# Optimization experiments

Measured on AMD Instinct MI355X. Metric: run time of the kernel, lower is better.

## Reference

```python
import jax, jax.numpy as jnp
import numpy as np

N, E = 50000, 800000
IN, EIN, HID, OUT = 128, 64, 256, 256
L, H = 3, 4
D = HID // H  # per-head out_feats


def setup_inputs() -> dict:
    key = jax.random.key(0)
    ks = jax.random.split(key, 20)
    s = 0.02
    return {
        "h": jax.random.normal(ks[0], (N, IN), jnp.float32),
        "efeat": jax.random.normal(ks[1], (E, EIN), jnp.float32),
        "src": jax.random.randint(ks[2], (E,), 0, N, jnp.int32),
        "dst": jax.random.randint(ks[3], (E,), 0, N, jnp.int32),
        "enc_w": jax.random.normal(ks[4], (IN, HID), jnp.float32) * s,
        "enc_b": jnp.zeros((HID,), jnp.float32),
        "eenc_w": jax.random.normal(ks[5], (EIN, HID), jnp.float32) * s,
        "eenc_b": jnp.zeros((HID,), jnp.float32),
        "Wn": jax.random.normal(ks[6], (L, HID, HID), jnp.float32) * s,
        "We": jax.random.normal(ks[7], (L, HID, HID), jnp.float32) * s,
        "al": jax.random.normal(ks[8], (L, H, D), jnp.float32) * s,
        "ar": jax.random.normal(ks[9], (L, H, D), jnp.float32) * s,
        "ae": jax.random.normal(ks[10], (L, H, D), jnp.float32) * s,
        "ln_g": jnp.ones((L, HID), jnp.float32),
        "ln_b": jnp.zeros((L, HID), jnp.float32),
        "out_w": jax.random.normal(ks[11], (HID, OUT), jnp.float32) * s,
        "out_b": jnp.zeros((OUT,), jnp.float32),
    }


def reference(h, efeat, src, dst, enc_w, enc_b, eenc_w, eenc_b,
              Wn, We, al, ar, ae, ln_g, ln_b, out_w, out_b):
    # Dropout layers act as identity (eval mode).
    n = h.shape[0]
    x = h @ enc_w + enc_b                      # [N, HID] node encoder
    ef = efeat @ eenc_w + eenc_b               # [E, HID] edge encoder
    nl, nh, nd = al.shape
    for l in range(nl):
        res = x
        feat = (x @ Wn[l]).reshape(n, nh, nd)          # [N,H,D]
        eft = (ef @ We[l]).reshape(-1, nh, nd)         # [E,H,D]
        el = jnp.sum(feat * al[l], axis=-1)            # [N,H]
        er = jnp.sum(feat * ar[l], axis=-1)            # [N,H]
        ee = jnp.sum(eft * ae[l], axis=-1)             # [E,H]
        e = jax.nn.leaky_relu(el[src] + er[dst] + ee, 0.2)  # [E,H]
        # edge softmax over incoming edges of each dst node
        m = jax.lax.stop_gradient(jax.ops.segment_max(e, dst, num_segments=n))
        a = jnp.exp(e - m[dst])
        ssum = jax.ops.segment_sum(a, dst, num_segments=n)
        alpha = a / ssum[dst]                          # [E,H]
        agg = jax.ops.segment_sum(alpha[:, :, None] * feat[src], dst,
                                  num_segments=n)      # [N,H,D]
        x = jax.nn.relu(agg.reshape(n, nh * nd))
        y = x + res
        mu = jnp.mean(y, axis=-1, keepdims=True)
        var = jnp.var(y, axis=-1, keepdims=True)
        x = (y - mu) / jnp.sqrt(var + 1e-5) * ln_g[l] + ln_b[l]
    return x @ out_w + out_b
```

## Files before the change

kernel.cpp:

```cpp
#include <hip/hip_runtime.h>
#include <math.h>


typedef __attribute__((ext_vector_type(8))) short bf16x8;
typedef __attribute__((ext_vector_type(4))) float f32x4;

__device__ __forceinline__ ushort f2b(float f) {
    unsigned u; __builtin_memcpy(&u, &f, 4);
    unsigned r = u + 0x7FFF + ((u >> 16) & 1);
    return (ushort)(r >> 16);
}
__device__ __forceinline__ float b2f(ushort u) {
    unsigned x = (unsigned)u << 16;
    float f; __builtin_memcpy(&f, &x, 4);
    return f;
}

__global__ void k_deg(const int* __restrict__ dst, int* __restrict__ deg, int E) {
    int e = blockIdx.x * 256 + threadIdx.x;
    if (e < E) atomicAdd(&deg[dst[e]], 1);
}

__global__ void k_bsum(const int* __restrict__ deg, int* __restrict__ bsum, int n) {
    __shared__ int wsum[4];
    int tid = threadIdx.x;
    int idx = blockIdx.x * 1024 + tid * 4;
    int4 v = make_int4(0, 0, 0, 0);
    if (idx + 3 < n) v = *(const int4*)(deg + idx);
    else {
        if (idx + 0 < n) v.x = deg[idx + 0];
        if (idx + 1 < n) v.y = deg[idx + 1];
        if (idx + 2 < n) v.z = deg[idx + 2];
    }
    int s = v.x + v.y + v.z + v.w;
#pragma unroll
    for (int off = 32; off; off >>= 1) s += __shfl_down(s, off, 64);
    if ((tid & 63) == 0) wsum[tid >> 6] = s;
    __syncthreads();
    if (tid == 0) bsum[blockIdx.x] = wsum[0] + wsum[1] + wsum[2] + wsum[3];
}

__global__ void k_bscan(const int* __restrict__ bsum, int* __restrict__ boff,
                        int* __restrict__ rowp, int NB, int n) {
    int tid = threadIdx.x;
    int v = (tid < NB) ? bsum[tid] : 0;
    int sc = v;
#pragma unroll
    for (int off = 1; off < 64; off <<= 1) {
        int t = __shfl_up(sc, off, 64);
        if ((tid & 63) >= off) sc += t;
    }
    if (tid < NB) boff[tid] = sc - v;
    if (tid == 63) rowp[n] = sc;
}

__global__ void k_bwrite(const int* __restrict__ deg, const int* __restrict__ boff,
                         int* __restrict__ rowp, int* __restrict__ cursor, int n) {
    __shared__ int wsum[4];
    __shared__ int woff_sh[4];
    int tid = threadIdx.x;
    int lane = tid & 63, wid = tid >> 6;
    int idx = blockIdx.x * 1024 + tid * 4;
    int4 v = make_int4(0, 0, 0, 0);
    if (idx + 3 < n) v = *(const int4*)(deg + idx);
    else {
        if (idx + 0 < n) v.x = deg[idx + 0];
        if (idx + 1 < n) v.y = deg[idx + 1];
        if (idx + 2 < n) v.z = deg[idx + 2];
    }
    int sum4 = v.x + v.y + v.z + v.w;
    int sc = sum4;
#pragma unroll
    for (int off = 1; off < 64; off <<= 1) {
        int t = __shfl_up(sc, off, 64);
        if (lane >= off) sc += t;
    }
    if (lane == 63) wsum[wid] = sc;
    __syncthreads();
    if (tid < 4) {
        int o = 0;
        for (int w = 0; w < tid; w++) o += wsum[w];
        woff_sh[tid] = o;
    }
    __syncthreads();
    int ex = boff[blockIdx.x] + woff_sh[wid] + (sc - sum4);
    int p0 = ex, p1 = ex + v.x, p2 = p1 + v.y, p3 = p2 + v.z;
    if (idx + 0 < n) { rowp[idx + 0] = p0; cursor[idx + 0] = p0; }
    if (idx + 1 < n) { rowp[idx + 1] = p1; cursor[idx + 1] = p1; }
    if (idx + 2 < n) { rowp[idx + 2] = p2; cursor[idx + 2] = p2; }
    if (idx + 3 < n) { rowp[idx + 3] = p3; cursor[idx + 3] = p3; }
}

__global__ void k_scatter(const int* __restrict__ dst, const int* __restrict__ src,
                          int* __restrict__ cursor, int* __restrict__ eid,
                          int* __restrict__ esrc, int E) {
    int e = blockIdx.x * 256 + threadIdx.x;
    if (e < E) {
        int pos = atomicAdd(&cursor[dst[e]], 1);
        eid[pos] = e;
        esrc[pos] = src[e];
    }
}

__global__ void k_ew(const float* __restrict__ We, const float* __restrict__ ae,
                     float* __restrict__ ew) {
    int t = blockIdx.x * 256 + threadIdx.x;
    if (t >= 3072) return;
    int l = t >> 10, r = t & 1023;
    int k = r >> 2, h = r & 3;
    const float* w = We + (size_t)l * 65536 + (size_t)k * 256 + h * 64;
    const float* a = ae + l * 256 + h * 64;
    float s = 0.f;
    for (int d = 0; d < 64; d++) s += w[d] * a[d];
    ew[t] = s;
}

__global__ void k_eew(const float* __restrict__ eenc_w, const float* __restrict__ eenc_b,
                      const float* __restrict__ ew, float* __restrict__ eew2,
                      float* __restrict__ eeb) {
    int t = blockIdx.x * 256 + threadIdx.x;
    if (t < 768) {
        int j = t / 12, lh = t % 12;
        int l = lh >> 2, h = lh & 3;
        float s = 0.f;
        for (int k = 0; k < 256; k++) s += eenc_w[j * 256 + k] * ew[l * 1024 + k * 4 + h];
        eew2[j * 12 + lh] = s;
    } else if (t < 780) {
        int lh = t - 768;
        int l = lh >> 2, h = lh & 3;
        float s = 0.f;
        for (int k = 0; k < 256; k++) s += eenc_b[k] * ew[l * 1024 + k * 4 + h];
        eeb[lh] = s;
    }
}

__global__ __launch_bounds__(256) void k_ee(const float* __restrict__ efeat,
                                            const float* __restrict__ eew2,
                                            const float* __restrict__ eeb,
                                            float* __restrict__ ee_l,
                                            int E) {
    const int tid = threadIdx.x;
    const int lane = tid & 63;
    const int wave = tid >> 6;
    const int q = lane & 15;
    const int sub = lane >> 4;

    float Wreg[4][12];
#pragma unroll
    for (int u = 0; u < 4; u++)
#pragma unroll
        for (int t = 0; t < 12; t++) Wreg[u][t] = eew2[(q * 4 + u) * 12 + t];
    float Bv[12];
#pragma unroll
    for (int t = 0; t < 12; t++) Bv[t] = eeb[t];

    const int base = blockIdx.x * 64 + wave * 16;
#pragma unroll
    for (int p = 0; p < 4; p++) {
        int e = base + p * 4 + sub;
        if (e >= E) return;
        float4 v = *(const float4*)(efeat + (size_t)e * 64 + q * 4);
        float acc[12];
#pragma unroll
        for (int t = 0; t < 12; t++)
            acc[t] = v.x * Wreg[0][t] + v.y * Wreg[1][t] + v.z * Wreg[2][t] +
                     v.w * Wreg[3][t];
#pragma unroll
        for (int m = 1; m < 16; m <<= 1)
#pragma unroll
            for (int t = 0; t < 12; t++) acc[t] += __shfl_xor(acc[t], m, 64);
        if (q == 0) {
#pragma unroll
            for (int l = 0; l < 3; l++) {
                float4 o = make_float4(acc[l * 4 + 0] + Bv[l * 4 + 0],
                                       acc[l * 4 + 1] + Bv[l * 4 + 1],
                                       acc[l * 4 + 2] + Bv[l * 4 + 2],
                                       acc[l * 4 + 3] + Bv[l * 4 + 3]);
                *(float4*)(ee_l + (size_t)l * E * 4 + (size_t)e * 4) = o;
            }
        }
    }
}

__global__ void k_f2b(const float* __restrict__ in, ushort* __restrict__ out, int n4) {
    int i = blockIdx.x * 256 + threadIdx.x;
    if (i >= n4) return;
    float4 v = *(const float4*)(in + (size_t)i * 4);
    ushort4 o;
    o.x = f2b(v.x); o.y = f2b(v.y); o.z = f2b(v.z); o.w = f2b(v.w);
    *(ushort4*)(out + (size_t)i * 4) = o;
}

__global__ void k_tr(const float* __restrict__ in, ushort* __restrict__ out, int K, int Nn) {
    int t = blockIdx.x * 256 + threadIdx.x;
    if (t >= K * Nn) return;
    int nn = t / K, k = t % K;
    out[t] = f2b(in[(size_t)k * Nn + nn]);
}

template <int KTILES, bool BIAS, bool STORE_F32, bool STORE_BF16>
__global__ __launch_bounds__(256) void gemm_mfma(const ushort* __restrict__ A,
                                                 const ushort* __restrict__ BT,
                                                 const float* __restrict__ bias,
                                                 float* __restrict__ Cf,
                                                 ushort* __restrict__ Cb, int M) {
    constexpr int K = KTILES * 32;
    __shared__ __align__(16) ushort As[128 * 32];
    __shared__ __align__(16) ushort Bs[128 * 32];
    const int tid = threadIdx.x;
    const int wave = tid >> 6;
    const int lane = tid & 63;
    const int rowBase = blockIdx.x * 128;
    const int colBase = blockIdx.y * 128;
    const int sRow = lane >> 2;
    const int sCol = (lane & 3) * 8;
    const int c0 = wave * 2, c1 = wave * 2 + 1;

    const ushort* gA0 = A + (size_t)(rowBase + c0 * 16 + sRow) * K + sCol;
    const ushort* gA1 = A + (size_t)(rowBase + c1 * 16 + sRow) * K + sCol;
    const ushort* gB0 = BT + (size_t)(colBase + c0 * 16 + sRow) * K + sCol;
    const ushort* gB1 = BT + (size_t)(colBase + c1 * 16 + sRow) * K + sCol;
    ushort* lA0 = As + c0 * 512;
    ushort* lA1 = As + c1 * 512;
    ushort* lB0 = Bs + c0 * 512;
    ushort* lB1 = Bs + c1 * 512;

    f32x4 acc[4][4] = {};
    const int wr = (wave >> 1) * 64, wc = (wave & 1) * 64;
    const int ml = lane & 15, q = lane >> 4;

    for (int kt = 0; kt < KTILES; ++kt) {
        __builtin_amdgcn_global_load_lds(
            (const __attribute__((address_space(1))) unsigned*)(gA0 + kt * 32),
            (__attribute__((address_space(3))) unsigned*)lA0, 16, 0, 0);
        __builtin_amdgcn_global_load_lds(
            (const __attribute__((address_space(1))) unsigned*)(gA1 + kt * 32),
            (__attribute__((address_space(3))) unsigned*)lA1, 16, 0, 0);
        __builtin_amdgcn_global_load_lds(
            (const __attribute__((address_space(1))) unsigned*)(gB0 + kt * 32),
            (__attribute__((address_space(3))) unsigned*)lB0, 16, 0, 0);
        __builtin_amdgcn_global_load_lds(
            (const __attribute__((address_space(1))) unsigned*)(gB1 + kt * 32),
            (__attribute__((address_space(3))) unsigned*)lB1, 16, 0, 0);
        __syncthreads();
        bf16x8 af[4], bfr[4];
#pragma unroll
        for (int i = 0; i < 4; i++)
            af[i] = *(const bf16x8*)&As[(wr + i * 16 + ml) * 32 + q * 8];
#pragma unroll
        for (int j = 0; j < 4; j++)
            bfr[j] = *(const bf16x8*)&Bs[(wc + j * 16 + ml) * 32 + q * 8];
#pragma unroll
        for (int i = 0; i < 4; i++)
#pragma unroll
            for (int j = 0; j < 4; j++)
                acc[i][j] = __builtin_amdgcn_mfma_f32_16x16x32_bf16(af[i], bfr[j], acc[i][j],
                                                                    0, 0, 0);
        __syncthreads();
    }

#pragma unroll
    for (int j = 0; j < 4; j++) {
        const int col = colBase + wc + j * 16 + ml;
        const float bb = BIAS ? bias[col] : 0.f;
#pragma unroll
        for (int i = 0; i < 4; i++) {
#pragma unroll
            for (int r = 0; r < 4; r++) {
                const int row = rowBase + wr + i * 16 + q * 4 + r;
                if (row < M) {
                    float v = acc[i][j][r] + bb;
                    if (STORE_F32) Cf[(size_t)row * 256 + col] = v;
                    if (STORE_BF16) Cb[(size_t)row * 256 + col] = f2b(v);
                }
            }
        }
    }
}

__global__ __launch_bounds__(256) void k_elr(const ushort* __restrict__ feat,
                                             const float* __restrict__ al,
                                             const float* __restrict__ ar,
                                             float* __restrict__ el,
                                             float* __restrict__ er, int N) {
    int lane = threadIdx.x & 63;
    int n = blockIdx.x * 4 + (threadIdx.x >> 6);
    if (n >= N) return;
    ushort4 f4 = *(const ushort4*)&feat[(size_t)n * 256 + lane * 4];
    float4 a4 = *(const float4*)&al[lane * 4];
    float4 r4 = *(const float4*)&ar[lane * 4];
    float f0 = b2f(f4.x), f1 = b2f(f4.y), f2 = b2f(f4.z), f3 = b2f(f4.w);
    float va = f0 * a4.x + f1 * a4.y + f2 * a4.z + f3 * a4.w;
    float vr = f0 * r4.x + f1 * r4.y + f2 * r4.z + f3 * r4.w;
#pragma unroll
    for (int m = 1; m < 16; m <<= 1) {
        va += __shfl_xor(va, m, 64);
        vr += __shfl_xor(vr, m, 64);
    }
    if ((lane & 15) == 0) {
        int h = lane >> 4;
        el[n * 4 + h] = va;
        er[n * 4 + h] = vr;
    }
}

__global__ __launch_bounds__(128) void k_agg(const int* __restrict__ rowp,
                                             const int* __restrict__ eid,
                                             const int* __restrict__ esrc,
                                             const float* __restrict__ ee,
                                             const float* __restrict__ el,
                                             const float* __restrict__ er,
                                             const ushort* __restrict__ feat,
                                             float* __restrict__ x_io,
                                             ushort* __restrict__ xb,
                                             const float* __restrict__ g,
                                             const float* __restrict__ b) {
    const int n = blockIdx.x;
    const int t = threadIdx.x;
    const int start = rowp[n], end = rowp[n + 1];
    __shared__ float w_sh[64][4];
    __shared__ int src_sh[64];
    __shared__ float redA[64][4];

    float ern[4];
    if (t < 64) {
        float4 e4 = *(const float4*)(er + (size_t)n * 4);
        ern[0] = e4.x; ern[1] = e4.y; ern[2] = e4.z; ern[3] = e4.w;
    }
    float wsum[4] = {0.f, 0.f, 0.f, 0.f};
    float acc[4] = {0.f, 0.f, 0.f, 0.f};
    const int half = t >> 6;
    const int tc = t & 63;
    const int h = tc >> 4;

    for (int cs = start; cs < end; cs += 64) {
        if (t < 64 && cs + t < end) {
            int pos = cs + t;
            int e = eid[pos];
            int s = esrc[pos];
            src_sh[t] = s;
            float4 elv = *(const float4*)(el + (size_t)s * 4);
            float4 eev = *(const float4*)(ee + (size_t)e * 4);
            float elva[4] = {elv.x, elv.y, elv.z, elv.w};
            float eeva[4] = {eev.x, eev.y, eev.z, eev.w};
#pragma unroll
            for (int hh = 0; hh < 4; hh++) {
                float sc = elva[hh] + ern[hh] + eeva[hh];
                sc = (sc > 0.f) ? sc : 0.2f * sc;
                float w = __expf(sc);
                w_sh[t][hh] = w;
                wsum[hh] += w;
            }
        }
        __syncthreads();
        int cnt = min(64, end - cs);
        for (int j = half; j < cnt; j += 2) {
            float w = w_sh[j][h];
            ushort4 p = *(const ushort4*)&feat[(size_t)src_sh[j] * 256 + tc * 4];
            acc[0] += w * b2f(p.x);
            acc[1] += w * b2f(p.y);
            acc[2] += w * b2f(p.z);
            acc[3] += w * b2f(p.w);
        }
        __syncthreads();
    }

    if (t >= 64) {
        redA[tc][0] = acc[0]; redA[tc][1] = acc[1];
        redA[tc][2] = acc[2]; redA[tc][3] = acc[3];
    }
    __syncthreads();
    if (t < 64) {
        acc[0] += redA[t][0]; acc[1] += redA[t][1];
        acc[2] += redA[t][2]; acc[3] += redA[t][3];
#pragma unroll
        for (int m = 1; m < 64; m <<= 1)
#pragma unroll
            for (int hh = 0; hh < 4; hh++) wsum[hh] += __shfl_xor(wsum[hh], m, 64);
        float y[4];
        float4 xr = *(const float4*)&x_io[(size_t)n * 256 + t * 4];
        float xra[4] = {xr.x, xr.y, xr.z, xr.w};
        float inv = (end > start) ? 1.f / wsum[h] : 0.f;
#pragma unroll
        for (int u = 0; u < 4; u++) {
            float v = fmaxf(acc[u] * inv, 0.f);
            y[u] = v + xra[u];
        }
        float s1 = y[0] + y[1] + y[2] + y[3];
        float s2 = y[0] * y[0] + y[1] * y[1] + y[2] * y[2] + y[3] * y[3];
#pragma unroll
        for (int m = 1; m < 64; m <<= 1) {
            s1 += __shfl_xor(s1, m, 64);
            s2 += __shfl_xor(s2, m, 64);
        }
        float mu = s1 * (1.f / 256.f);
        float var = s2 * (1.f / 256.f) - mu * mu;
        float rstd = rsqrtf(var + 1e-5f);
        float4 gv = *(const float4*)&g[t * 4];
        float4 bv = *(const float4*)&b[t * 4];
        float ga[4] = {gv.x, gv.y, gv.z, gv.w};
        float ba[4] = {bv.x, bv.y, bv.z, bv.w};
        float o[4];
        ushort4 ob;
#pragma unroll
        for (int u = 0; u < 4; u++) o[u] = (y[u] - mu) * rstd * ga[u] + ba[u];
        ob.x = f2b(o[0]); ob.y = f2b(o[1]); ob.z = f2b(o[2]); ob.w = f2b(o[3]);
        *(float4*)&x_io[(size_t)n * 256 + t * 4] = make_float4(o[0], o[1], o[2], o[3]);
        *(ushort4*)&xb[(size_t)n * 256 + t * 4] = ob;
    }
}

extern "C" void kernel_launch(void* const* d_in, const int* in_sizes, int n_in,
                              void* d_out, int out_size, void* d_ws, size_t ws_size,
                              hipStream_t stream) {
    const float* h      = (const float*)d_in[0];
    const float* efeat  = (const float*)d_in[1];
    const int*   src    = (const int*)d_in[2];
    const int*   dst    = (const int*)d_in[3];
    const float* enc_w  = (const float*)d_in[4];
    const float* enc_b  = (const float*)d_in[5];
    const float* eenc_w = (const float*)d_in[6];
    const float* eenc_b = (const float*)d_in[7];
    const float* Wn     = (const float*)d_in[8];
    const float* We     = (const float*)d_in[9];
    const float* al     = (const float*)d_in[10];
    const float* ar     = (const float*)d_in[11];
    const float* ae     = (const float*)d_in[12];
    const float* ln_g   = (const float*)d_in[13];
    const float* ln_b   = (const float*)d_in[14];
    const float* out_w  = (const float*)d_in[15];
    const float* out_b  = (const float*)d_in[16];

    const int N = in_sizes[0] / 128;
    const int E = in_sizes[2];
    const int Mpad = ((N + 127) / 128) * 128;
    const int NB = (N + 1023) / 1024;

    char* ws = (char*)d_ws;
    size_t off = 0;
    auto alloc = [&](size_t bytes) -> char* {
        char* p = ws + off;
        off += (bytes + 255) & ~(size_t)255;
        return p;
    };
    float*  X      = (float*)alloc((size_t)Mpad * 256 * 4);
    ushort* Xb     = (ushort*)alloc((size_t)Mpad * 256 * 2);
    ushort* F      = (ushort*)alloc((size_t)Mpad * 256 * 2);
    ushort* hb     = (ushort*)alloc((size_t)Mpad * 128 * 2);
    float*  el     = (float*)alloc((size_t)N * 4 * 4);
    float*  er     = (float*)alloc((size_t)N * 4 * 4);
    float*  ee_l   = (float*)alloc((size_t)E * 12 * 4);
    int*    esrc   = (int*)alloc((size_t)E * 4);
    int*    eid    = (int*)alloc((size_t)E * 4);
    int*    deg    = (int*)alloc((size_t)N * 4);
    int*    rowp   = (int*)alloc((size_t)(N + 1) * 4);
    int*    cursor = (int*)alloc((size_t)N * 4);
    int*    bsum   = (int*)alloc(64 * 4);
    int*    boff   = (int*)alloc(64 * 4);
    float*  ew     = (float*)alloc(3072 * 4);
    float*  eew2   = (float*)alloc(768 * 4);
    float*  eeb    = (float*)alloc(64);
    ushort* encT   = (ushort*)alloc(256 * 128 * 2);
    ushort* WnT    = (ushort*)alloc(3 * 256 * 256 * 2);
    ushort* outT   = (ushort*)alloc(256 * 256 * 2);
    (void)ws_size; (void)n_in; (void)out_size;

    hipMemsetAsync(deg, 0, (size_t)N * 4, stream);
    k_deg<<<(E + 255) / 256, 256, 0, stream>>>(dst, deg, E);
    k_bsum<<<NB, 256, 0, stream>>>(deg, bsum, N);
    k_bscan<<<1, 64, 0, stream>>>(bsum, boff, rowp, NB, N);
    k_bwrite<<<NB, 256, 0, stream>>>(deg, boff, rowp, cursor, N);
    k_scatter<<<(E + 255) / 256, 256, 0, stream>>>(dst, src, cursor, eid, esrc, E);

    k_ew<<<12, 256, 0, stream>>>(We, ae, ew);
    k_eew<<<4, 256, 0, stream>>>(eenc_w, eenc_b, ew, eew2, eeb);
    k_ee<<<(E + 63) / 64, 256, 0, stream>>>(efeat, eew2, eeb, ee_l, E);

    k_f2b<<<(N * 128 / 4 + 255) / 256, 256, 0, stream>>>(h, hb, N * 128 / 4);
    k_tr<<<(128 * 256 + 255) / 256, 256, 0, stream>>>(enc_w, encT, 128, 256);
    for (int l = 0; l < 3; l++)
        k_tr<<<(256 * 256 + 255) / 256, 256, 0, stream>>>(Wn + (size_t)l * 65536,
                                                          WnT + (size_t)l * 65536, 256, 256);
    k_tr<<<(256 * 256 + 255) / 256, 256, 0, stream>>>(out_w, outT, 256, 256);

    dim3 gG(Mpad / 128, 2);
    gemm_mfma<4, true, true, true><<<gG, 256, 0, stream>>>(hb, encT, enc_b, X, Xb, N);

    for (int l = 0; l < 3; l++) {
        gemm_mfma<8, false, false, true><<<gG, 256, 0, stream>>>(
            Xb, WnT + (size_t)l * 65536, nullptr, nullptr, F, N);
        k_elr<<<(N + 3) / 4, 256, 0, stream>>>(F, al + l * 256, ar + l * 256, el, er, N);
        k_agg<<<N, 128, 0, stream>>>(rowp, eid, esrc, ee_l + (size_t)l * E * 4, el, er,
                                     F, X, Xb, ln_g + l * 256, ln_b + l * 256);
    }
    gemm_mfma<8, true, true, false><<<gG, 256, 0, stream>>>(Xb, outT, out_b,
                                                            (float*)d_out, nullptr, N);
}
```

Measured before the change: 932.2 us.

## Widen aggregation gathers to 16B, batch transposes, skip last-layer fp32 store

The aggregation kernel now has each thread gather 8 bf16 features (16-byte loads) across four edge streams instead of 4 features across two. Partials are reduced through shared memory and LayerNorm runs on 32 threads. The fp32 residual write is skipped on the final layer, since only the bf16 copy feeds the output GEMM. The weight transpose launches are merged into one kernel, and the edge-score kernel processes 8 lanes per edge with two float4 loads, halving the shuffle-reduction depth. These changes aim to cut memory instructions, launch overhead and redundant stores, but fewer threads end up doing the LayerNorm epilogue.

```diff
diff --git a/kernel.cpp b/kernel.cpp
--- a/kernel.cpp
+++ b/kernel.cpp
@@ -3,6 +3,7 @@
 
 
 typedef __attribute__((ext_vector_type(8))) short bf16x8;
+typedef __attribute__((ext_vector_type(8))) unsigned short u16x8;
 typedef __attribute__((ext_vector_type(4))) float f32x4;
 
 __device__ __forceinline__ ushort f2b(float f) {
@@ -142,31 +143,35 @@
     const int tid = threadIdx.x;
     const int lane = tid & 63;
     const int wave = tid >> 6;
-    const int q = lane & 15;
-    const int sub = lane >> 4;
-
-    float Wreg[4][12];
+    const int q = lane & 7;
+    const int g8 = lane >> 3;
+
+    float W[8][12];
 #pragma unroll
     for (int u = 0; u < 4; u++)
 #pragma unroll
-        for (int t = 0; t < 12; t++) Wreg[u][t] = eew2[(q * 4 + u) * 12 + t];
+        for (int t = 0; t < 12; t++) {
+            W[u][t]     = eew2[(q * 4 + u) * 12 + t];
+            W[u + 4][t] = eew2[(32 + q * 4 + u) * 12 + t];
+        }
     float Bv[12];
 #pragma unroll
     for (int t = 0; t < 12; t++) Bv[t] = eeb[t];
 
-    const int base = blockIdx.x * 64 + wave * 16;
+    const int base = blockIdx.x * 128 + wave * 32;
 #pragma unroll
     for (int p = 0; p < 4; p++) {
-        int e = base + p * 4 + sub;
+        int e = base + p * 8 + g8;
         if (e >= E) return;
-        float4 v = *(const float4*)(efeat + (size_t)e * 64 + q * 4);
+        float4 v0 = *(const float4*)(efeat + (size_t)e * 64 + q * 4);
+        float4 v1 = *(const float4*)(efeat + (size_t)e * 64 + 32 + q * 4);
         float acc[12];
 #pragma unroll
         for (int t = 0; t < 12; t++)
-            acc[t] = v.x * Wreg[0][t] + v.y * Wreg[1][t] + v.z * Wreg[2][t] +
-                     v.w * Wreg[3][t];
-#pragma unroll
-        for (int m = 1; m < 16; m <<= 1)
+            acc[t] = v0.x * W[0][t] + v0.y * W[1][t] + v0.z * W[2][t] + v0.w * W[3][t] +
+                     v1.x * W[4][t] + v1.y * W[5][t] + v1.z * W[6][t] + v1.w * W[7][t];
+#pragma unroll
+        for (int m = 1; m < 8; m <<= 1)
 #pragma unroll
             for (int t = 0; t < 12; t++) acc[t] += __shfl_xor(acc[t], m, 64);
         if (q == 0) {
@@ -191,11 +196,27 @@
     *(ushort4*)(out + (size_t)i * 4) = o;
 }
 
-__global__ void k_tr(const float* __restrict__ in, ushort* __restrict__ out, int K, int Nn) {
+__global__ void k_trs(const float* __restrict__ enc_w, const float* __restrict__ Wn,
+                      const float* __restrict__ out_w, ushort* __restrict__ encT,
+                      ushort* __restrict__ WnT, ushort* __restrict__ outT) {
     int t = blockIdx.x * 256 + threadIdx.x;
-    if (t >= K * Nn) return;
-    int nn = t / K, k = t % K;
-    out[t] = f2b(in[(size_t)k * Nn + nn]);
+    if (t < 32768) {
+        int nn = t >> 7, k = t & 127;
+        encT[t] = f2b(enc_w[k * 256 + nn]);
+        return;
+    }
+    t -= 32768;
+    if (t < 3 * 65536) {
+        int l = t >> 16, r = t & 65535;
+        int nn = r >> 8, k = r & 255;
+        WnT[(size_t)l * 65536 + r] = f2b(Wn[(size_t)l * 65536 + k * 256 + nn]);
+        return;
+    }
+    t -= 3 * 65536;
+    {
+        int nn = t >> 8, k = t & 255;
+        outT[t] = f2b(out_w[k * 256 + nn]);
+    }
 }
 
 template <int KTILES, bool BIAS, bool STORE_F32, bool STORE_BF16>
@@ -304,6 +325,7 @@
     }
 }
 
+template <bool WRITE_X>
 __global__ __launch_bounds__(128) void k_agg(const int* __restrict__ rowp,
                                              const int* __restrict__ eid,
                                              const int* __restrict__ esrc,
@@ -320,7 +342,7 @@
     const int start = rowp[n], end = rowp[n + 1];
     __shared__ float w_sh[64][4];
     __shared__ int src_sh[64];
-    __shared__ float redA[64][4];
+    __shared__ float redA[3][32][8];
 
     float ern[4];
     if (t < 64) {
@@ -328,10 +350,10 @@
         ern[0] = e4.x; ern[1] = e4.y; ern[2] = e4.z; ern[3] = e4.w;
     }
     float wsum[4] = {0.f, 0.f, 0.f, 0.f};
-    float acc[4] = {0.f, 0.f, 0.f, 0.f};
-    const int half = t >> 6;
-    const int tc = t & 63;
-    const int h = tc >> 4;
+    float acc[8] = {0.f, 0.f, 0.f, 0.f, 0.f, 0.f, 0.f, 0.f};
+    const int stream = t >> 5;
+    const int c = t & 31;
+    const int h = c >> 3;
 
     for (int cs = start; cs < end; cs += 64) {
         if (t < 64 && cs + t < end) {
@@ -354,59 +376,72 @@
         }
         __syncthreads();
         int cnt = min(64, end - cs);
-        for (int j = half; j < cnt; j += 2) {
+        for (int j = stream; j < cnt; j += 4) {
             float w = w_sh[j][h];
-            ushort4 p = *(const ushort4*)&feat[(size_t)src_sh[j] * 256 + tc * 4];
-            acc[0] += w * b2f(p.x);
-            acc[1] += w * b2f(p.y);
-            acc[2] += w * b2f(p.z);
-            acc[3] += w * b2f(p.w);
+            u16x8 p = *(const u16x8*)&feat[(size_t)src_sh[j] * 256 + c * 8];
+#pragma unroll
+            for (int u = 0; u < 8; u++) acc[u] += w * b2f((ushort)p[u]);
         }
         __syncthreads();
     }
 
-    if (t >= 64) {
-        redA[tc][0] = acc[0]; redA[tc][1] = acc[1];
-        redA[tc][2] = acc[2]; redA[tc][3] = acc[3];
+    if (stream > 0) {
+#pragma unroll
+        for (int u = 0; u < 8; u++) redA[stream - 1][c][u] = acc[u];
+    }
+    if (t < 64) {
+#pragma unroll
+        for (int m = 1; m < 64; m <<= 1)
+#pragma unroll
+            for (int hh = 0; hh < 4; hh++) wsum[hh] += __shfl_xor(wsum[hh], m, 64);
     }
     __syncthreads();
-    if (t < 64) {
-        acc[0] += redA[t][0]; acc[1] += redA[t][1];
-        acc[2] += redA[t][2]; acc[3] += redA[t][3];
-#pragma unroll
-        for (int m = 1; m < 64; m <<= 1)
-#pragma unroll
-            for (int hh = 0; hh < 4; hh++) wsum[hh] += __shfl_xor(wsum[hh], m, 64);
-        float y[4];
-        float4 xr = *(const float4*)&x_io[(size_t)n * 256 + t * 4];
-        float xra[4] = {xr.x, xr.y, xr.z, xr.w};
+    if (t < 32) {
+#pragma unroll
+        for (int ss = 0; ss < 3; ss++)
+#pragma unroll
+            for (int u = 0; u < 8; u++) acc[u] += redA[ss][c][u];
+        float4 xr0 = *(const float4*)&x_io[(size_t)n * 256 + c * 8];
+        float4 xr1 = *(const float4*)&x_io[(size_t)n * 256 + c * 8 + 4];
+        float xra[8] = {xr0.x, xr0.y, xr0.z, xr0.w, xr1.x, xr1.y, xr1.z, xr1.w};
         float inv = (end > start) ? 1.f / wsum[h] : 0.f;
-#pragma unroll
-        for (int u = 0; u < 4; u++) {
+        float y[8];
+        float s1 = 0.f, s2 = 0.f;
+#pragma unroll
+        for (int u = 0; u < 8; u++) {
             float v = fmaxf(acc[u] * inv, 0.f);
             y[u] = v + xra[u];
-        }
-        float s1 = y[0] + y[1] + y[2] + y[3];
-        float s2 = y[0] * y[0] + y[1] * y[1] + y[2] * y[2] + y[3] * y[3];
-#pragma unroll
-        for (int m = 1; m < 64; m <<= 1) {
+            s1 += y[u];
+            s2 += y[u] * y[u];
+        }
+#pragma unroll
+        for (int m = 1; m < 32; m <<= 1) {
             s1 += __shfl_xor(s1, m, 64);
             s2 += __shfl_xor(s2, m, 64);
         }
         float mu = s1 * (1.f / 256.f);
         float var = s2 * (1.f / 256.f) - mu * mu;
         float rstd = rsqrtf(var + 1e-5f);
-        float4 gv = *(const float4*)&g[t * 4];
-        float4 bv = *(const float4*)&b[t * 4];
-        float ga[4] = {gv.x, gv.y, gv.z, gv.w};
-        float ba[4] = {bv.x, bv.y, bv.z, bv.w};
-        float o[4];
-        ushort4 ob;
-#pragma unroll
-        for (int u = 0; u < 4; u++) o[u] = (y[u] - mu) * rstd * ga[u] + ba[u];
-        ob.x = f2b(o[0]); ob.y = f2b(o[1]); ob.z = f2b(o[2]); ob.w = f2b(o[3]);
-        *(float4*)&x_io[(size_t)n * 256 + t * 4] = make_float4(o[0], o[1], o[2], o[3]);
-        *(ushort4*)&xb[(size_t)n * 256 + t * 4] = ob;
+        float4 gv0 = *(const float4*)&g[c * 8];
+        float4 gv1 = *(const float4*)&g[c * 8 + 4];
+        float4 bv0 = *(const float4*)&b[c * 8];
+        float4 bv1 = *(const float4*)&b[c * 8 + 4];
+        float ga[8] = {gv0.x, gv0.y, gv0.z, gv0.w, gv1.x, gv1.y, gv1.z, gv1.w};
+        float ba[8] = {bv0.x, bv0.y, bv0.z, bv0.w, bv1.x, bv1.y, bv1.z, bv1.w};
+        float o[8];
+        u16x8 ob;
+#pragma unroll
+        for (int u = 0; u < 8; u++) {
+            o[u] = (y[u] - mu) * rstd * ga[u] + ba[u];
+            ob[u] = f2b(o[u]);
+        }
+        if (WRITE_X) {
+            *(float4*)&x_io[(size_t)n * 256 + c * 8] =
+                make_float4(o[0], o[1], o[2], o[3]);
+            *(float4*)&x_io[(size_t)n * 256 + c * 8 + 4] =
+                make_float4(o[4], o[5], o[6], o[7]);
+        }
+        *(u16x8*)&xb[(size_t)n * 256 + c * 8] = ob;
     }
 }
 
@@ -474,14 +509,11 @@
 
     k_ew<<<12, 256, 0, stream>>>(We, ae, ew);
     k_eew<<<4, 256, 0, stream>>>(eenc_w, eenc_b, ew, eew2, eeb);
-    k_ee<<<(E + 63) / 64, 256, 0, stream>>>(efeat, eew2, eeb, ee_l, E);
+    k_ee<<<(E + 127) / 128, 256, 0, stream>>>(efeat, eew2, eeb, ee_l, E);
 
     k_f2b<<<(N * 128 / 4 + 255) / 256, 256, 0, stream>>>(h, hb, N * 128 / 4);
-    k_tr<<<(128 * 256 + 255) / 256, 256, 0, stream>>>(enc_w, encT, 128, 256);
-    for (int l = 0; l < 3; l++)
-        k_tr<<<(256 * 256 + 255) / 256, 256, 0, stream>>>(Wn + (size_t)l * 65536,
-                                                          WnT + (size_t)l * 65536, 256, 256);
-    k_tr<<<(256 * 256 + 255) / 256, 256, 0, stream>>>(out_w, outT, 256, 256);
+    k_trs<<<(32768 + 4 * 65536 + 255) / 256, 256, 0, stream>>>(enc_w, Wn, out_w,
+                                                               encT, WnT, outT);
 
     dim3 gG(Mpad / 128, 2);
     gemm_mfma<4, true, true, true><<<gG, 256, 0, stream>>>(hb, encT, enc_b, X, Xb, N);
@@ -490,8 +522,14 @@
         gemm_mfma<8, false, false, true><<<gG, 256, 0, stream>>>(
             Xb, WnT + (size_t)l * 65536, nullptr, nullptr, F, N);
         k_elr<<<(N + 3) / 4, 256, 0, stream>>>(F, al + l * 256, ar + l * 256, el, er, N);
-        k_agg<<<N, 128, 0, stream>>>(rowp, eid, esrc, ee_l + (size_t)l * E * 4, el, er,
-                                     F, X, Xb, ln_g + l * 256, ln_b + l * 256);
+        if (l < 2)
+            k_agg<true><<<N, 128, 0, stream>>>(rowp, eid, esrc, ee_l + (size_t)l * E * 4,
+                                               el, er, F, X, Xb, ln_g + l * 256,
+                                               ln_b + l * 256);
+        else
+            k_agg<false><<<N, 128, 0, stream>>>(rowp, eid, esrc, ee_l + (size_t)l * E * 4,
+                                                el, er, F, X, Xb, ln_g + l * 256,
+                                                ln_b + l * 256);
     }
     gemm_mfma<8, true, true, false><<<gG, 256, 0, stream>>>(Xb, outT, out_b,
                                                             (float*)d_out, nullptr, N);
```

Result: faster. 886.9 us (-4.9%).
